# Kernel optimization log

Hardware: AMD Instinct MI355X
Metric: run time of the kernel (lower is better)

Reference implementation:

```python
import jax, jax.numpy as jnp
import numpy as np

B, S, C = 16, 4096, 512


def setup_inputs() -> dict:
    key = jax.random.key(0)
    k1, k2, k3 = jax.random.split(key, 3)
    tag_logits_batch = jax.random.normal(k1, (B, S, C), dtype=jnp.float32)
    # probabilistic targets: normalize uniform draws so rows sum to 1
    t = jax.random.uniform(k2, (B, S, C), dtype=jnp.float32)
    target = t / jnp.sum(t, axis=-1, keepdims=True)
    mask = jax.random.randint(k3, (B, S), 0, 2, dtype=jnp.int32)
    return {"tag_logits_batch": tag_logits_batch, "target": target, "mask": mask}


def reference(tag_logits_batch, target, mask):
    # Soft-label cross-entropy per token: -sum_y target_y * log_softmax(logits)_y
    logp = jax.nn.log_softmax(tag_logits_batch, axis=-1)        # [B,S,C]
    tok_loss = -jnp.sum(target * logp, axis=-1)                  # [B,S]
    m = (mask == 1).astype(tok_loss.dtype)                       # [B,S]
    cnt = jnp.sum(m, axis=1)                                     # [B]
    # mean over active tokens per batch element (reduction='mean')
    per_batch = jnp.sum(tok_loss * m, axis=1) / jnp.maximum(cnt, 1.0)
    # torch code skips batch rows with no active tokens, then means over the rest
    has = (cnt > 0).astype(per_batch.dtype)                      # [B]
    return jnp.sum(per_batch * has) / jnp.maximum(jnp.sum(has), 1.0)
```

## Files before the change

### kernel.cpp

```cpp
#include <hip/hip_runtime.h>
#include <hip/hip_bf16.h>

#define BB 16
#define SS 4096
#define CC 512
#define NTOK (BB * SS)
#define TOK_PER_WAVE 4
#define TOK_PER_BLOCK 16

__global__ __launch_bounds__(256) void tok_loss_kernel(
    const float* __restrict__ logits,
    const float* __restrict__ target,
    const int*   __restrict__ mask,
    float*       __restrict__ acc) {
    const int wave = threadIdx.x >> 6;
    const int lane = threadIdx.x & 63;
    const int tokbase = blockIdx.x * TOK_PER_BLOCK + wave * TOK_PER_WAVE;
    const int batch = tokbase / SS;

    const int4 mv = *(const int4*)(mask + tokbase);
    const int act[TOK_PER_WAVE] = {mv.x == 1, mv.y == 1, mv.z == 1, mv.w == 1};

    float se[TOK_PER_WAVE], dot[TOK_PER_WAVE];
    float cnt = 0.0f;
    #pragma unroll
    for (int i = 0; i < TOK_PER_WAVE; ++i) { se[i] = 0.0f; dot[i] = 0.0f; }

    #pragma unroll
    for (int i = 0; i < TOK_PER_WAVE; ++i) {
        if (act[i]) {
            cnt += 1.0f;
            const float4* xp = (const float4*)(logits + (size_t)(tokbase + i) * CC);
            const float4* tp = (const float4*)(target + (size_t)(tokbase + i) * CC);
            float4 x0 = xp[lane];
            float4 x1 = xp[lane + 64];
            float4 t0 = tp[lane];
            float4 t1 = tp[lane + 64];
            se[i] = __expf(x0.x) + __expf(x0.y) + __expf(x0.z) + __expf(x0.w)
                  + __expf(x1.x) + __expf(x1.y) + __expf(x1.z) + __expf(x1.w);
            dot[i] = t0.x * x0.x + t0.y * x0.y + t0.z * x0.z + t0.w * x0.w
                   + t1.x * x1.x + t1.y * x1.y + t1.z * x1.z + t1.w * x1.w;
        }
    }

    #pragma unroll
    for (int off = 32; off >= 1; off >>= 1) {
        #pragma unroll
        for (int i = 0; i < TOK_PER_WAVE; ++i) {
            se[i]  += __shfl_xor(se[i], off, 64);
            dot[i] += __shfl_xor(dot[i], off, 64);
        }
    }

    float loss = 0.0f;
    #pragma unroll
    for (int i = 0; i < TOK_PER_WAVE; ++i)
        if (act[i]) loss += __logf(se[i]) - dot[i];

    __shared__ float ls[4], lc[4];
    if (lane == 0) { ls[wave] = loss; lc[wave] = cnt; }
    __syncthreads();
    if (threadIdx.x == 0) {
        float L = ls[0] + ls[1] + ls[2] + ls[3];
        float C = lc[0] + lc[1] + lc[2] + lc[3];
        atomicAdd(&acc[2 * batch],     L);
        atomicAdd(&acc[2 * batch + 1], C);
    }
}

__global__ __launch_bounds__(64) void finalize_kernel(
    const float* __restrict__ acc,
    float*       __restrict__ out) {
    const int lane = threadIdx.x;
    float pb = 0.0f, has = 0.0f;
    if (lane < BB) {
        float s = acc[2 * lane];
        float c = acc[2 * lane + 1];
        if (c > 0.0f) { pb = s / c; has = 1.0f; }
    }
    #pragma unroll
    for (int off = 32; off >= 1; off >>= 1) {
        pb  += __shfl_xor(pb, off, 64);
        has += __shfl_xor(has, off, 64);
    }
    if (lane == 0) out[0] = pb / fmaxf(has, 1.0f);
}

extern "C" void kernel_launch(void* const* d_in, const int* in_sizes, int n_in,
                              void* d_out, int out_size, void* d_ws, size_t ws_size,
                              hipStream_t stream) {
    const float* logits = (const float*)d_in[0];
    const float* target = (const float*)d_in[1];
    const int*   mask   = (const int*)d_in[2];
    float* out = (float*)d_out;
    float* acc = (float*)d_ws;

    hipMemsetAsync(acc, 0, 2 * BB * sizeof(float), stream);
    tok_loss_kernel<<<NTOK / TOK_PER_BLOCK, 256, 0, stream>>>(logits, target, mask, acc);
    finalize_kernel<<<1, 64, 0, stream>>>(acc, out);
}
```

Before: 284.9 us.

## Give each wave a strided run of token pairs and drop mask-based load skipping

```diff
diff --git a/kernel.cpp b/kernel.cpp
--- a/kernel.cpp
+++ b/kernel.cpp
@@ -5,66 +5,69 @@
 #define SS 4096
 #define CC 512
 #define NTOK (BB * SS)
-#define TOK_PER_WAVE 4
-#define TOK_PER_BLOCK 16
+#define BLOCKS_PER_BATCH 64
+#define WAVES_PER_BATCH (BLOCKS_PER_BATCH * 4)
+#define TOKS_PER_WAVE (SS / WAVES_PER_BATCH)
+#define STEPS (TOKS_PER_WAVE / 2)
 
 __global__ __launch_bounds__(256) void tok_loss_kernel(
     const float* __restrict__ logits,
     const float* __restrict__ target,
     const int*   __restrict__ mask,
     float*       __restrict__ acc) {
-    const int wave = threadIdx.x >> 6;
-    const int lane = threadIdx.x & 63;
-    const int tokbase = blockIdx.x * TOK_PER_BLOCK + wave * TOK_PER_WAVE;
-    const int batch = tokbase / SS;
+    const int wave  = threadIdx.x >> 6;
+    const int lane  = threadIdx.x & 63;
+    const int batch = blockIdx.x / BLOCKS_PER_BATCH;
+    const int wib   = (blockIdx.x % BLOCKS_PER_BATCH) * 4 + wave;
 
-    const int4 mv = *(const int4*)(mask + tokbase);
-    const int act[TOK_PER_WAVE] = {mv.x == 1, mv.y == 1, mv.z == 1, mv.w == 1};
-
-    float se[TOK_PER_WAVE], dot[TOK_PER_WAVE];
-    float cnt = 0.0f;
-    #pragma unroll
-    for (int i = 0; i < TOK_PER_WAVE; ++i) { se[i] = 0.0f; dot[i] = 0.0f; }
+    float lossAcc = 0.0f;
+    float cntAcc  = 0.0f;
 
     #pragma unroll
-    for (int i = 0; i < TOK_PER_WAVE; ++i) {
-        if (act[i]) {
-            cnt += 1.0f;
-            const float4* xp = (const float4*)(logits + (size_t)(tokbase + i) * CC);
-            const float4* tp = (const float4*)(target + (size_t)(tokbase + i) * CC);
-            float4 x0 = xp[lane];
-            float4 x1 = xp[lane + 64];
-            float4 t0 = tp[lane];
-            float4 t1 = tp[lane + 64];
-            se[i] = __expf(x0.x) + __expf(x0.y) + __expf(x0.z) + __expf(x0.w)
-                  + __expf(x1.x) + __expf(x1.y) + __expf(x1.z) + __expf(x1.w);
-            dot[i] = t0.x * x0.x + t0.y * x0.y + t0.z * x0.z + t0.w * x0.w
-                   + t1.x * x1.x + t1.y * x1.y + t1.z * x1.z + t1.w * x1.w;
+    for (int j = 0; j < STEPS; ++j) {
+        const int tokA = batch * SS + j * (WAVES_PER_BATCH * 2) + 2 * wib;
+        const int tokB = tokA + 1;
+
+        const float mA = (mask[tokA] == 1) ? 1.0f : 0.0f;
+        const float mB = (mask[tokB] == 1) ? 1.0f : 0.0f;
+
+        const float4* xpA = (const float4*)(logits + (size_t)tokA * CC);
+        const float4* tpA = (const float4*)(target + (size_t)tokA * CC);
+        const float4* xpB = (const float4*)(logits + (size_t)tokB * CC);
+        const float4* tpB = (const float4*)(target + (size_t)tokB * CC);
+        float4 xA0 = xpA[lane];
+        float4 xA1 = xpA[lane + 64];
+        float4 xB0 = xpB[lane];
+        float4 xB1 = xpB[lane + 64];
+        float4 tA0 = tpA[lane];
+        float4 tA1 = tpA[lane + 64];
+        float4 tB0 = tpB[lane];
+        float4 tB1 = tpB[lane + 64];
+
+        float seA = __expf(xA0.x) + __expf(xA0.y) + __expf(xA0.z) + __expf(xA0.w)
+                  + __expf(xA1.x) + __expf(xA1.y) + __expf(xA1.z) + __expf(xA1.w);
+        float seB = __expf(xB0.x) + __expf(xB0.y) + __expf(xB0.z) + __expf(xB0.w)
+                  + __expf(xB1.x) + __expf(xB1.y) + __expf(xB1.z) + __expf(xB1.w);
+        float dotA = tA0.x * xA0.x + tA0.y * xA0.y + tA0.z * xA0.z + tA0.w * xA0.w
+                   + tA1.x * xA1.x + tA1.y * xA1.y + tA1.z * xA1.z + tA1.w * xA1.w;
+        float dotB = tB0.x * xB0.x + tB0.y * xB0.y + tB0.z * xB0.z + tB0.w * xB0.w
+                   + tB1.x * xB1.x + tB1.y * xB1.y + tB1.z * xB1.z + tB1.w * xB1.w;
+
+        #pragma unroll
+        for (int off = 32; off >= 1; off >>= 1) {
+            seA  += __shfl_xor(seA, off, 64);
+            seB  += __shfl_xor(seB, off, 64);
+            dotA += __shfl_xor(dotA, off, 64);
+            dotB += __shfl_xor(dotB, off, 64);
         }
+
+        lossAcc += mA * (__logf(seA) - dotA) + mB * (__logf(seB) - dotB);
+        cntAcc  += mA + mB;
     }
 
-    #pragma unroll
-    for (int off = 32; off >= 1; off >>= 1) {
-        #pragma unroll
-        for (int i = 0; i < TOK_PER_WAVE; ++i) {
-            se[i]  += __shfl_xor(se[i], off, 64);
-            dot[i] += __shfl_xor(dot[i], off, 64);
-        }
-    }
-
-    float loss = 0.0f;
-    #pragma unroll
-    for (int i = 0; i < TOK_PER_WAVE; ++i)
-        if (act[i]) loss += __logf(se[i]) - dot[i];
-
-    __shared__ float ls[4], lc[4];
-    if (lane == 0) { ls[wave] = loss; lc[wave] = cnt; }
-    __syncthreads();
-    if (threadIdx.x == 0) {
-        float L = ls[0] + ls[1] + ls[2] + ls[3];
-        float C = lc[0] + lc[1] + lc[2] + lc[3];
-        atomicAdd(&acc[2 * batch],     L);
-        atomicAdd(&acc[2 * batch + 1], C);
+    if (lane == 0) {
+        atomicAdd(&acc[2 * batch],     lossAcc);
+        atomicAdd(&acc[2 * batch + 1], cntAcc);
     }
 }
 
@@ -96,6 +99,6 @@
     float* acc = (float*)d_ws;
 
     hipMemsetAsync(acc, 0, 2 * BB * sizeof(float), stream);
-    tok_loss_kernel<<<NTOK / TOK_PER_BLOCK, 256, 0, stream>>>(logits, target, mask, acc);
+    tok_loss_kernel<<<BB * BLOCKS_PER_BATCH, 256, 0, stream>>>(logits, target, mask, acc);
     finalize_kernel<<<1, 64, 0, stream>>>(acc, out);
 }
```

Measured after the change: 320.0 us. 1.12x slower.

## Compact active tokens first, then stream them with persistent prefetching waves

Applied to the files above, without the earlier changes.

```diff
diff --git a/kernel.cpp b/kernel.cpp
--- a/kernel.cpp
+++ b/kernel.cpp
@@ -5,66 +5,99 @@
 #define SS 4096
 #define CC 512
 #define NTOK (BB * SS)
-#define TOK_PER_WAVE 4
-#define TOK_PER_BLOCK 16
+#define LOSS_BLOCKS 2048
+#define WAVES_TOTAL (LOSS_BLOCKS * 4)
+#define WPB (WAVES_TOTAL / BB)
 
-__global__ __launch_bounds__(256) void tok_loss_kernel(
+
+__global__ __launch_bounds__(256) void compact_kernel(
+    const int* __restrict__ mask,
+    int*       __restrict__ idxbuf,
+    int*       __restrict__ cursors,
+    float*     __restrict__ acc) {
+    const int t     = blockIdx.x * 256 + threadIdx.x;
+    const int batch = blockIdx.x / 16;
+    const int lane  = threadIdx.x & 63;
+    const int wave  = threadIdx.x >> 6;
+
+    const bool active = (mask[t] == 1);
+    unsigned long long ball = __ballot(active);
+    const int prefix = __popcll(ball & ((1ull << lane) - 1ull));
+    const int wcount = __popcll(ball);
+
+    __shared__ int wbase[4];
+    __shared__ int blockbase;
+    if (lane == 0) wbase[wave] = wcount;
+    __syncthreads();
+    if (threadIdx.x == 0) {
+        int total = wbase[0] + wbase[1] + wbase[2] + wbase[3];
+        blockbase = atomicAdd(&cursors[batch], total);
+        atomicAdd(&acc[2 * batch + 1], (float)total);
+        int s = 0;
+        for (int i = 0; i < 4; ++i) { int c = wbase[i]; wbase[i] = s; s += c; }
+    }
+    __syncthreads();
+    if (active)
+        idxbuf[batch * SS + blockbase + wbase[wave] + prefix] = t;
+}
+
+__global__ __launch_bounds__(256, 8) void loss_kernel(
     const float* __restrict__ logits,
     const float* __restrict__ target,
-    const int*   __restrict__ mask,
+    const int*   __restrict__ idxbuf,
+    const int*   __restrict__ cursors,
     float*       __restrict__ acc) {
-    const int wave = threadIdx.x >> 6;
-    const int lane = threadIdx.x & 63;
-    const int tokbase = blockIdx.x * TOK_PER_BLOCK + wave * TOK_PER_WAVE;
-    const int batch = tokbase / SS;
+    const int wave  = threadIdx.x >> 6;
+    const int lane  = threadIdx.x & 63;
+    const int wid   = blockIdx.x * 4 + wave;
+    const int batch = wid & (BB - 1);
+    const int w2    = wid >> 4;
+    const int cnt   = cursors[batch];
+    const int* list = idxbuf + batch * SS;
 
-    const int4 mv = *(const int4*)(mask + tokbase);
-    const int act[TOK_PER_WAVE] = {mv.x == 1, mv.y == 1, mv.z == 1, mv.w == 1};
+    float dotAcc = 0.0f;
+    float logAcc = 0.0f;
 
-    float se[TOK_PER_WAVE], dot[TOK_PER_WAVE];
-    float cnt = 0.0f;
-    #pragma unroll
-    for (int i = 0; i < TOK_PER_WAVE; ++i) { se[i] = 0.0f; dot[i] = 0.0f; }
-
-    #pragma unroll
-    for (int i = 0; i < TOK_PER_WAVE; ++i) {
-        if (act[i]) {
-            cnt += 1.0f;
-            const float4* xp = (const float4*)(logits + (size_t)(tokbase + i) * CC);
-            const float4* tp = (const float4*)(target + (size_t)(tokbase + i) * CC);
-            float4 x0 = xp[lane];
-            float4 x1 = xp[lane + 64];
-            float4 t0 = tp[lane];
-            float4 t1 = tp[lane + 64];
-            se[i] = __expf(x0.x) + __expf(x0.y) + __expf(x0.z) + __expf(x0.w)
-                  + __expf(x1.x) + __expf(x1.y) + __expf(x1.z) + __expf(x1.w);
-            dot[i] = t0.x * x0.x + t0.y * x0.y + t0.z * x0.z + t0.w * x0.w
-                   + t1.x * x1.x + t1.y * x1.y + t1.z * x1.z + t1.w * x1.w;
+    int k = w2;
+    bool have = (k < cnt);
+    float4 x0, x1, t0, t1;
+    if (have) {
+        const int tok = list[k];
+        const float4* xp = (const float4*)(logits + (size_t)tok * CC);
+        const float4* tp = (const float4*)(target + (size_t)tok * CC);
+        x0 = xp[lane]; x1 = xp[lane + 64];
+        t0 = tp[lane]; t1 = tp[lane + 64];
+    }
+    while (have) {
+        const int kn = k + WPB;
+        const bool haveN = (kn < cnt);
+        float4 nx0, nx1, nt0, nt1;
+        if (haveN) {
+            const int tokN = list[kn];
+            const float4* xp = (const float4*)(logits + (size_t)tokN * CC);
+            const float4* tp = (const float4*)(target + (size_t)tokN * CC);
+            nx0 = xp[lane]; nx1 = xp[lane + 64];
+            nt0 = tp[lane]; nt1 = tp[lane + 64];
         }
+        float se = __expf(x0.x) + __expf(x0.y) + __expf(x0.z) + __expf(x0.w)
+                 + __expf(x1.x) + __expf(x1.y) + __expf(x1.z) + __expf(x1.w);
+        dotAcc += t0.x * x0.x + t0.y * x0.y + t0.z * x0.z + t0.w * x0.w
+                + t1.x * x1.x + t1.y * x1.y + t1.z * x1.z + t1.w * x1.w;
+        #pragma unroll
+        for (int off = 32; off >= 1; off >>= 1)
+            se += __shfl_xor(se, off, 64);
+        logAcc += __logf(se);
+        x0 = nx0; x1 = nx1; t0 = nt0; t1 = nt1;
+        k = kn; have = haveN;
     }
 
     #pragma unroll
-    for (int off = 32; off >= 1; off >>= 1) {
-        #pragma unroll
-        for (int i = 0; i < TOK_PER_WAVE; ++i) {
-            se[i]  += __shfl_xor(se[i], off, 64);
-            dot[i] += __shfl_xor(dot[i], off, 64);
-        }
-    }
+    for (int off = 32; off >= 1; off >>= 1)
+        dotAcc += __shfl_xor(dotAcc, off, 64);
 
-    float loss = 0.0f;
-    #pragma unroll
-    for (int i = 0; i < TOK_PER_WAVE; ++i)
-        if (act[i]) loss += __logf(se[i]) - dot[i];
-
-    __shared__ float ls[4], lc[4];
-    if (lane == 0) { ls[wave] = loss; lc[wave] = cnt; }
-    __syncthreads();
-    if (threadIdx.x == 0) {
-        float L = ls[0] + ls[1] + ls[2] + ls[3];
-        float C = lc[0] + lc[1] + lc[2] + lc[3];
-        atomicAdd(&acc[2 * batch],     L);
-        atomicAdd(&acc[2 * batch + 1], C);
+    if (lane == 0) {
+        float contrib = logAcc - dotAcc;
+        if (contrib != 0.0f) atomicAdd(&acc[2 * batch], contrib);
     }
 }
 
@@ -92,10 +125,13 @@
     const float* logits = (const float*)d_in[0];
     const float* target = (const float*)d_in[1];
     const int*   mask   = (const int*)d_in[2];
-    float* out = (float*)d_out;
-    float* acc = (float*)d_ws;
+    float* out     = (float*)d_out;
+    float* acc     = (float*)d_ws;
+    int*   cursors = (int*)((char*)d_ws + 128);
+    int*   idxbuf  = (int*)((char*)d_ws + 256);
 
-    hipMemsetAsync(acc, 0, 2 * BB * sizeof(float), stream);
-    tok_loss_kernel<<<NTOK / TOK_PER_BLOCK, 256, 0, stream>>>(logits, target, mask, acc);
+    hipMemsetAsync(d_ws, 0, 192, stream);
+    compact_kernel<<<NTOK / 256, 256, 0, stream>>>(mask, idxbuf, cursors, acc);
+    loss_kernel<<<LOSS_BLOCKS, 256, 0, stream>>>(logits, target, idxbuf, cursors, acc);
     finalize_kernel<<<1, 64, 0, stream>>>(acc, out);
 }
```

Result: slower. 292.6 us (+2.7%).
